# Optimization experiments

Hardware: AMD Instinct MI355X
Metric: run time of the kernel (lower is better)

## Reference

```python
import jax, jax.numpy as jnp
import numpy as np


def apply_rope(x):
    # x: [B, T, H, D]
    T, D = x.shape[1], x.shape[3]
    inv_freq = 1.0 / (10000.0 ** (jnp.arange(0, D, 2, dtype=jnp.float32) / D))  # [D/2]
    t = jnp.arange(T, dtype=jnp.float32)
    freqs = jnp.outer(t, inv_freq)  # [T, D/2]
    sin_f = jnp.sin(freqs)[None, :, None, :]
    cos_f = jnp.cos(freqs)[None, :, None, :]
    x1, x2 = jnp.split(x, 2, axis=-1)
    return jnp.concatenate([x1 * cos_f - x2 * sin_f, x1 * sin_f + x2 * cos_f], axis=-1)


def setup_inputs() -> dict:
    key = jax.random.key(0)
    ks = jax.random.split(key, 5)
    B, T, D = 8, 8192, 128
    s = 1.0 / np.sqrt(D)
    return {
        "x": jax.random.normal(ks[0], (B, T, D), dtype=jnp.float32),
        "Wq": jax.random.normal(ks[1], (D, D), dtype=jnp.float32) * s,
        "bq": jnp.zeros((D,), dtype=jnp.float32),
        "Wk": jax.random.normal(ks[2], (D, D), dtype=jnp.float32) * s,
        "bk": jnp.zeros((D,), dtype=jnp.float32),
        "Wv": jax.random.normal(ks[3], (D, D), dtype=jnp.float32) * s,
        "bv": jnp.zeros((D,), dtype=jnp.float32),
        "Wo": jax.random.normal(ks[4], (D, D), dtype=jnp.float32) * s,
        "bo": jnp.zeros((D,), dtype=jnp.float32),
    }


def reference(x, Wq, bq, Wk, bk, Wv, bv, Wo, bo):
    n_heads = 8
    B, T, d_model = x.shape
    head_dim = d_model // n_heads

    q = (x @ Wq + bq).reshape(B, T, n_heads, head_dim)
    k = (x @ Wk + bk).reshape(B, T, n_heads, head_dim)
    v = (x @ Wv + bv).reshape(B, T, n_heads, head_dim)

    q = jax.nn.elu(apply_rope(q)) + 1.0
    k = jax.nn.elu(apply_rope(k)) + 1.0

    # non-causal linear attention: context = sum_t k_t v_t^T per head
    context = jnp.einsum("bthd,bthe->bhde", k, v)            # [B,H,Dh,Dh]
    out = jnp.einsum("bthd,bhde->bthe", q, context)           # [B,T,H,Dh]
    k_sum = jnp.sum(k, axis=1)                                  # [B,H,Dh]
    z = 1.0 / (jnp.einsum("bthd,bhd->bth", q, k_sum) + 1e-6)  # [B,T,H]
    out = out * z[..., None]

    out = out.reshape(B, T, d_model)
    return out @ Wo + bo
```

## Files before the change

### kernel.cpp

```cpp
#include <hip/hip_runtime.h>
#include <hip/hip_bf16.h>


typedef __attribute__((ext_vector_type(8))) short short8;
typedef __attribute__((ext_vector_type(4))) float floatx4;

#define DEV __device__ __forceinline__
#define MFMA __builtin_amdgcn_mfma_f32_16x16x32_bf16

DEV unsigned short bfh(float f) {
  unsigned int x = __float_as_uint(f);
  x += 0x7fffu + ((x >> 16) & 1u);
  return (unsigned short)(x >> 16);
}
DEV float bfdec(unsigned short u) { return __uint_as_float(((unsigned int)u) << 16); }
DEV void splitf(float f, unsigned short& h, unsigned short& l) {
  h = bfh(f);
  l = bfh(f - bfdec(h));
}

DEV void xpose_frag(floatx4 m0, floatx4 m1, int lane16, int quad,
                    short8& hi, short8& lo) {
  union { short8 s; unsigned short u[8]; } H, L;
#pragma unroll
  for (int j = 0; j < 8; ++j) {
    int srcLane = lane16 + (((quad & 1) * 2 + (j >> 2)) << 4);
    float vA = __shfl(m0[j & 3], srcLane, 64);
    float vB = __shfl(m1[j & 3], srcLane, 64);
    float v = (quad < 2) ? vA : vB;
    splitf(v, H.u[j], L.u[j]);
  }
  hi = H.s; lo = L.s;
}

__global__ void k_prep(const float* __restrict__ Wq, const float* __restrict__ Wk,
                       const float* __restrict__ Wv,
                       unsigned short* __restrict__ WTh, unsigned short* __restrict__ WTl,
                       float* __restrict__ ctxz, float2* __restrict__ ropeT) {
  int gid = blockIdx.x * 256 + threadIdx.x;
  if (gid < 6144) {
    int mat = gid >> 11, r = gid & 2047, n = r >> 4, k0 = (r & 15) * 8;
    const float* W = (mat == 0) ? Wq : (mat == 1) ? Wk : Wv;
    union { uint4 q; unsigned short u[8]; } oh, ol;
#pragma unroll
    for (int i = 0; i < 8; ++i) splitf(W[(size_t)(k0 + i) * 128 + n], oh.u[i], ol.u[i]);
    *(uint4*)&WTh[mat * 16384 + n * 128 + k0] = oh.q;
    *(uint4*)&WTl[mat * 16384 + n * 128 + k0] = ol.q;
  } else if (gid < 6144 + 17408) {
    ctxz[gid - 6144] = 0.0f;
  } else if (gid < 6144 + 17408 + 65536) {
    int r = gid - 23552;
    int t = r >> 3, j = r & 7;
    float invf = 1.0f / powf(10000.0f, (float)j * 0.125f);
    float s, c;
    sincosf((float)t * invf, &s, &c);
    ropeT[r] = make_float2(c, s);
  }
}

__global__ __launch_bounds__(512) void k_qkv(
    const float* __restrict__ x, const float2* __restrict__ ropeT,
    const unsigned short* __restrict__ WTh, const unsigned short* __restrict__ WTl,
    const float* __restrict__ bq, const float* __restrict__ bk, const float* __restrict__ bv,
    float* __restrict__ ctx, float* __restrict__ ksum,
    unsigned short* __restrict__ qws) {
  __shared__ unsigned short xh[64 * 136];
  __shared__ float rc[64][9], rs[64][9];
  const int tid = threadIdx.x;
  const int row0 = blockIdx.x * 64;
  const int b = row0 >> 13;
  const int t0 = row0 & 8191;

  {
    int r = tid >> 3, j = tid & 7;
    float2 cs = ropeT[(t0 + r) * 8 + j];
    rc[r][j] = cs.x; rs[r][j] = cs.y;
  }
  {
    int r = tid >> 3, cg = (tid & 7) * 16;
    const float* xp = x + (size_t)(row0 + r) * 128 + cg;
    float4 a = *(const float4*)xp;
    float4 b4 = *(const float4*)(xp + 4);
    float4 c4 = *(const float4*)(xp + 8);
    float4 d4 = *(const float4*)(xp + 12);
    float v[16] = {a.x, a.y, a.z, a.w, b4.x, b4.y, b4.z, b4.w,
                   c4.x, c4.y, c4.z, c4.w, d4.x, d4.y, d4.z, d4.w};
    union { short8 s; unsigned short u[8]; } h0, h1;
#pragma unroll
    for (int i = 0; i < 8; ++i) { h0.u[i] = bfh(v[i]); h1.u[i] = bfh(v[8 + i]); }
    *(short8*)&xh[r * 136 + cg] = h0.s;
    *(short8*)&xh[r * 136 + cg + 8] = h1.s;
  }
  __syncthreads();

  const int l = tid & 63, w = tid >> 6;
  const int lane16 = l & 15, quad = l >> 4;

  floatx4 acc[3][4];
#pragma unroll
  for (int i = 0; i < 3; ++i)
#pragma unroll
    for (int j = 0; j < 4; ++j) acc[i][j] = (floatx4){0.f, 0.f, 0.f, 0.f};

  size_t wbase[3];
#pragma unroll
  for (int mat = 0; mat < 3; ++mat)
    wbase[mat] = (size_t)mat * 16384 + (size_t)(w * 16 + lane16) * 128 + quad * 8;

  short8 wh[2][3], wl[2][3];
#pragma unroll
  for (int mat = 0; mat < 3; ++mat) {
    wh[0][mat] = *(const short8*)(WTh + wbase[mat]);
    wl[0][mat] = *(const short8*)(WTl + wbase[mat]);
  }

#pragma unroll
  for (int ks = 0; ks < 4; ++ks) {
    const int cur = ks & 1, nxt = cur ^ 1;
    if (ks < 3) {
#pragma unroll
      for (int mat = 0; mat < 3; ++mat) {
        wh[nxt][mat] = *(const short8*)(WTh + wbase[mat] + (ks + 1) * 32);
        wl[nxt][mat] = *(const short8*)(WTl + wbase[mat] + (ks + 1) * 32);
      }
    }
    short8 afh[4];
#pragma unroll
    for (int mt = 0; mt < 4; ++mt)
      afh[mt] = *(const short8*)&xh[(mt * 16 + lane16) * 136 + ks * 32 + quad * 8];
#pragma unroll
    for (int mat = 0; mat < 3; ++mat) {
#pragma unroll
      for (int mt = 0; mt < 4; ++mt) {
        acc[mat][mt] = MFMA(afh[mt], wh[cur][mat], acc[mat][mt], 0, 0, 0);
        acc[mat][mt] = MFMA(afh[mt], wl[cur][mat], acc[mat][mt], 0, 0, 0);
      }
    }
  }

  {
    int col = w * 16 + lane16;
    float bias[3] = {bq[col], bk[col], bv[col]};
#pragma unroll
    for (int mat = 0; mat < 3; ++mat)
#pragma unroll
      for (int mt = 0; mt < 4; ++mt)
#pragma unroll
        for (int r = 0; r < 4; ++r) acc[mat][mt][r] += bias[mat];
  }

  {
    const int d = lane16, j = d & 7;
#pragma unroll
    for (int mt = 0; mt < 4; ++mt) {
      float cc[4], ss[4];
#pragma unroll
      for (int r = 0; r < 4; ++r) {
        int tl = mt * 16 + quad * 4 + r;
        cc[r] = rc[tl][j]; ss[r] = rs[tl][j];
      }
#pragma unroll
      for (int mat = 0; mat < 2; ++mat) {
#pragma unroll
        for (int r = 0; r < 4; ++r) {
          float v = acc[mat][mt][r];
          float p = __shfl_xor(v, 8);
          float nv = (d < 8) ? (v * cc[r] - p * ss[r]) : (p * ss[r] + v * cc[r]);
          acc[mat][mt][r] = (nv > 0.f) ? (nv + 1.f) : __expf(nv);
        }
      }
    }
  }
  __syncthreads();

  unsigned short* qS = xh;
#pragma unroll
  for (int mt = 0; mt < 4; ++mt)
#pragma unroll
    for (int r = 0; r < 4; ++r)
      qS[(mt * 16 + quad * 4 + r) * 136 + w * 16 + lane16] = bfh(acc[0][mt][r]);

  {
    float s = 0.f;
#pragma unroll
    for (int mt = 0; mt < 4; ++mt)
#pragma unroll
      for (int r = 0; r < 4; ++r) s += acc[1][mt][r];
    s += __shfl_xor(s, 16);
    s += __shfl_xor(s, 32);
    if (l < 16) atomicAdd(&ksum[(b * 8 + w) * 16 + lane16], s);
  }

  {
    floatx4 c = (floatx4){0.f, 0.f, 0.f, 0.f};
#pragma unroll
    for (int ks2 = 0; ks2 < 2; ++ks2) {
      short8 kh, kl, vh, vl;
      xpose_frag(acc[1][ks2 * 2], acc[1][ks2 * 2 + 1], lane16, quad, kh, kl);
      xpose_frag(acc[2][ks2 * 2], acc[2][ks2 * 2 + 1], lane16, quad, vh, vl);
      c = MFMA(kh, vh, c, 0, 0, 0);
      c = MFMA(kl, vh, c, 0, 0, 0);
      c = MFMA(kh, vl, c, 0, 0, 0);
    }
#pragma unroll
    for (int r = 0; r < 4; ++r)
      atomicAdd(&ctx[((size_t)(b * 8 + w) * 16 + quad * 4 + r) * 16 + lane16], c[r]);
  }
  __syncthreads();

  {
    int r = tid >> 3, c = (tid & 7) * 16;
    uint4 a0 = *(const uint4*)&qS[r * 136 + c];
    uint4 a1 = *(const uint4*)&qS[r * 136 + c + 8];
    *(uint4*)&qws[(size_t)(row0 + r) * 128 + c] = a0;
    *(uint4*)&qws[(size_t)(row0 + r) * 128 + c + 8] = a1;
  }
}

__global__ __launch_bounds__(512) void k_zout(
    const unsigned short* __restrict__ qws,
    const float* __restrict__ Wo, const float* __restrict__ bo,
    const float* __restrict__ ctx, const float* __restrict__ ksum,
    float* __restrict__ out) {
  __shared__ __align__(16) unsigned short mh[16384], ml[16384];
  __shared__ float ctxS[2048];
  __shared__ float ksumS[128], boS[128];
  const int tid = threadIdx.x;
  const int row0 = blockIdx.x * 128;
  const int b = row0 >> 13;
  const int l = tid & 63, w = tid >> 6;
  const int lane16 = l & 15, quad = l >> 4;

  {
    float4 c4 = *(const float4*)(ctx + (size_t)b * 2048 + tid * 4);
    *(float4*)&ctxS[tid * 4] = c4;
  }
  if (tid < 128) ksumS[tid] = ksum[b * 128 + tid];
  else if (tid < 256) boS[tid - 128] = bo[tid - 128];
  __syncthreads();

  {
    int oc = tid & 127;
    int qcg0 = (tid >> 7) * 4;
#pragma unroll
    for (int hh = 0; hh < 2; ++hh) {
      int h = (qcg0 >> 1) + hh;
      float m0[8] = {0, 0, 0, 0, 0, 0, 0, 0};
      float m1[8] = {0, 0, 0, 0, 0, 0, 0, 0};
#pragma unroll 4
      for (int e = 0; e < 16; ++e) {
        float wv = Wo[(size_t)(h * 16 + e) * 128 + oc];
        const float* cp = ctxS + h * 256 + e;
#pragma unroll
        for (int i = 0; i < 8; ++i) {
          m0[i] += cp[i * 16] * wv;
          m1[i] += cp[(8 + i) * 16] * wv;
        }
      }
#pragma unroll
      for (int half = 0; half < 2; ++half) {
        int qcg = qcg0 + hh * 2 + half;
        const float* mm = half ? m1 : m0;
        union { uint4 q; unsigned short u[8]; } oh, ol;
#pragma unroll
        for (int i = 0; i < 8; ++i) splitf(mm[i], oh.u[i], ol.u[i]);
        int grp = (((oc >> 4) * 4 + (qcg >> 2)) * 64) + (qcg & 3) * 16 + (oc & 15);
        *(uint4*)&mh[grp * 8] = oh.q;
        *(uint4*)&ml[grp * 8] = ol.q;
      }
    }
  }
  __syncthreads();

  const int trow = row0 + w * 16 + lane16;
  short8 ah[4], al[4];
#pragma unroll
  for (int ks = 0; ks < 4; ++ks) {
    union { short8 s8; unsigned short u[8]; } qq;
    qq.s8 = *(const short8*)&qws[(size_t)trow * 128 + ks * 32 + quad * 8];
    int kb = ks * 32 + quad * 8;
    float s = 0.f;
#pragma unroll
    for (int j = 0; j < 8; ++j) s += bfdec(qq.u[j]) * ksumS[kb + j];
    s += __shfl_xor(s, 16);
    float z = 1.0f / (s + 1e-6f);
    union { short8 s8; unsigned short u[8]; } H, L;
#pragma unroll
    for (int j = 0; j < 8; ++j) splitf(bfdec(qq.u[j]) * z, H.u[j], L.u[j]);
    ah[ks] = H.s8;
    al[ks] = L.s8;
  }

  floatx4 oacc[8];
#pragma unroll
  for (int j = 0; j < 8; ++j) oacc[j] = (floatx4){0.f, 0.f, 0.f, 0.f};

#pragma unroll
  for (int nt = 0; nt < 8; ++nt) {
#pragma unroll
    for (int ks = 0; ks < 4; ++ks) {
      int moff = ((nt * 4 + ks) * 64 + l) * 8;
      short8 wbh = *(const short8*)&mh[moff];
      short8 wbl = *(const short8*)&ml[moff];
      oacc[nt] = MFMA(ah[ks], wbh, oacc[nt], 0, 0, 0);
      oacc[nt] = MFMA(al[ks], wbh, oacc[nt], 0, 0, 0);
      oacc[nt] = MFMA(ah[ks], wbl, oacc[nt], 0, 0, 0);
    }
  }
  __syncthreads();

  float* outW = (float*)((char*)mh + w * 8192);
#pragma unroll
  for (int nt = 0; nt < 8; ++nt) {
    float bb = boS[nt * 16 + lane16];
#pragma unroll
    for (int r = 0; r < 4; ++r)
      outW[(quad * 4 + r) * 128 + nt * 16 + lane16] = oacc[nt][r] + bb;
  }
  __syncthreads();

  {
    int rr = l >> 2, c0 = (l & 3) * 4;
#pragma unroll
    for (int j = 0; j < 8; ++j) {
      float4 v4 = *(const float4*)&outW[rr * 128 + c0 + j * 16];
      *(float4*)&out[(size_t)(row0 + w * 16 + rr) * 128 + c0 + j * 16] = v4;
    }
  }
}

extern "C" void kernel_launch(void* const* d_in, const int* in_sizes, int n_in,
                              void* d_out, int out_size, void* d_ws, size_t ws_size,
                              hipStream_t stream) {
  const float* x  = (const float*)d_in[0];
  const float* Wq = (const float*)d_in[1];
  const float* bq = (const float*)d_in[2];
  const float* Wk = (const float*)d_in[3];
  const float* bk = (const float*)d_in[4];
  const float* Wv = (const float*)d_in[5];
  const float* bv = (const float*)d_in[6];
  const float* Wo = (const float*)d_in[7];
  const float* bo = (const float*)d_in[8];
  float* out = (float*)d_out;

  unsigned short* qws = (unsigned short*)d_ws;
  unsigned short* WTh = qws + 8388608;
  unsigned short* WTl = WTh + 49152;
  float* ctx  = (float*)(WTl + 49152);
  float* ksum = ctx + 16384;
  float2* ropeT = (float2*)(ksum + 1024);

  k_prep<<<348, 256, 0, stream>>>(Wq, Wk, Wv, WTh, WTl, ctx, ropeT);
  k_qkv<<<1024, 512, 0, stream>>>(x, ropeT, WTh, WTl, bq, bk, bv, ctx, ksum, qws);
  k_zout<<<512, 512, 0, stream>>>(qws, Wo, bo, ctx, ksum, out);
}
```

Measured before the change: 164.0 us.

## Fuse QKV and output kernels into one cooperative kernel with grid barrier

Merges the QKV/context kernel and the output-projection kernel into one cooperatively launched kernel of 256 blocks. Each block handles 256 rows in four 64-row tiles. Q is kept in shared memory rather than written to a bf16 workspace and read back, and ctx/ksum partials are accumulated in registers across tiles, so each block issues one set of atomics. A global atomic barrier separates the context reduction from the output phase. In exchange, grid parallelism is reduced, tiles are processed serially, shared memory use grows, and the code now depends on cooperative launch and the barrier counter being zeroed by k_prep.

Result: slower. 229.8 us (+40.1%).

```diff
diff --git a/kernel.cpp b/kernel.cpp
--- a/kernel.cpp
+++ b/kernel.cpp
@@ -46,10 +46,10 @@
     for (int i = 0; i < 8; ++i) splitf(W[(size_t)(k0 + i) * 128 + n], oh.u[i], ol.u[i]);
     *(uint4*)&WTh[mat * 16384 + n * 128 + k0] = oh.q;
     *(uint4*)&WTl[mat * 16384 + n * 128 + k0] = ol.q;
-  } else if (gid < 6144 + 17408) {
+  } else if (gid < 6144 + 17424) {
     ctxz[gid - 6144] = 0.0f;
-  } else if (gid < 6144 + 17408 + 65536) {
-    int r = gid - 23552;
+  } else if (gid < 6144 + 17424 + 65536) {
+    int r = gid - 23568;
     int t = r >> 3, j = r & 7;
     float invf = 1.0f / powf(10000.0f, (float)j * 0.125f);
     float s, c;
@@ -58,185 +58,174 @@
   }
 }
 
-__global__ __launch_bounds__(512) void k_qkv(
+__global__ __launch_bounds__(512, 2) void k_main(
     const float* __restrict__ x, const float2* __restrict__ ropeT,
     const unsigned short* __restrict__ WTh, const unsigned short* __restrict__ WTl,
     const float* __restrict__ bq, const float* __restrict__ bk, const float* __restrict__ bv,
-    float* __restrict__ ctx, float* __restrict__ ksum,
-    unsigned short* __restrict__ qws) {
-  __shared__ unsigned short xh[64 * 136];
-  __shared__ float rc[64][9], rs[64][9];
+    const float* __restrict__ Wo, const float* __restrict__ bo,
+    float* __restrict__ ctx, float* __restrict__ ksum, unsigned int* __restrict__ bar,
+    float* __restrict__ out) {
+  __shared__ unsigned short qS[256 * 136];
+  __shared__ union {
+    struct { unsigned short xh[64 * 136]; float rc[64][9]; float rs[64][9]; } p1;
+    struct { unsigned short mh[16384], ml[16384];
+             float ctxS[2048], ksumS[128], boS[128]; } p2;
+  } U;
   const int tid = threadIdx.x;
-  const int row0 = blockIdx.x * 64;
+  const int row0 = blockIdx.x * 256;
   const int b = row0 >> 13;
-  const int t0 = row0 & 8191;
-
-  {
-    int r = tid >> 3, j = tid & 7;
-    float2 cs = ropeT[(t0 + r) * 8 + j];
-    rc[r][j] = cs.x; rs[r][j] = cs.y;
-  }
-  {
-    int r = tid >> 3, cg = (tid & 7) * 16;
-    const float* xp = x + (size_t)(row0 + r) * 128 + cg;
-    float4 a = *(const float4*)xp;
-    float4 b4 = *(const float4*)(xp + 4);
-    float4 c4 = *(const float4*)(xp + 8);
-    float4 d4 = *(const float4*)(xp + 12);
-    float v[16] = {a.x, a.y, a.z, a.w, b4.x, b4.y, b4.z, b4.w,
-                   c4.x, c4.y, c4.z, c4.w, d4.x, d4.y, d4.z, d4.w};
-    union { short8 s; unsigned short u[8]; } h0, h1;
-#pragma unroll
-    for (int i = 0; i < 8; ++i) { h0.u[i] = bfh(v[i]); h1.u[i] = bfh(v[8 + i]); }
-    *(short8*)&xh[r * 136 + cg] = h0.s;
-    *(short8*)&xh[r * 136 + cg + 8] = h1.s;
-  }
-  __syncthreads();
-
   const int l = tid & 63, w = tid >> 6;
   const int lane16 = l & 15, quad = l >> 4;
 
-  floatx4 acc[3][4];
-#pragma unroll
-  for (int i = 0; i < 3; ++i)
-#pragma unroll
-    for (int j = 0; j < 4; ++j) acc[i][j] = (floatx4){0.f, 0.f, 0.f, 0.f};
-
-  size_t wbase[3];
-#pragma unroll
-  for (int mat = 0; mat < 3; ++mat)
-    wbase[mat] = (size_t)mat * 16384 + (size_t)(w * 16 + lane16) * 128 + quad * 8;
-
-  short8 wh[2][3], wl[2][3];
-#pragma unroll
-  for (int mat = 0; mat < 3; ++mat) {
-    wh[0][mat] = *(const short8*)(WTh + wbase[mat]);
-    wl[0][mat] = *(const short8*)(WTl + wbase[mat]);
-  }
-
-#pragma unroll
-  for (int ks = 0; ks < 4; ++ks) {
-    const int cur = ks & 1, nxt = cur ^ 1;
-    if (ks < 3) {
-#pragma unroll
-      for (int mat = 0; mat < 3; ++mat) {
-        wh[nxt][mat] = *(const short8*)(WTh + wbase[mat] + (ks + 1) * 32);
-        wl[nxt][mat] = *(const short8*)(WTl + wbase[mat] + (ks + 1) * 32);
-      }
-    }
-    short8 afh[4];
+  short8 wfh[4][3], wfl[4][3];
+#pragma unroll
+  for (int ks = 0; ks < 4; ++ks)
+#pragma unroll
+    for (int mat = 0; mat < 3; ++mat) {
+      size_t off = (size_t)mat * 16384 + (size_t)(w * 16 + lane16) * 128 + ks * 32 + quad * 8;
+      wfh[ks][mat] = *(const short8*)(WTh + off);
+      wfl[ks][mat] = *(const short8*)(WTl + off);
+    }
+  const int col = w * 16 + lane16;
+  const float biasq = bq[col], biask = bk[col], biasv = bv[col];
+
+  float ksum_acc = 0.f;
+  floatx4 ctxc = (floatx4){0.f, 0.f, 0.f, 0.f};
+
+#pragma unroll 1
+  for (int tile = 0; tile < 4; ++tile) {
+    const int trow0 = row0 + tile * 64;
+    const int t0 = trow0 & 8191;
+    {
+      int r = tid >> 3, j = tid & 7;
+      float2 cs = ropeT[(t0 + r) * 8 + j];
+      U.p1.rc[r][j] = cs.x; U.p1.rs[r][j] = cs.y;
+    }
+    {
+      int r = tid >> 3, cg = (tid & 7) * 16;
+      const float* xp = x + (size_t)(trow0 + r) * 128 + cg;
+      float4 a = *(const float4*)xp;
+      float4 b4 = *(const float4*)(xp + 4);
+      float4 c4 = *(const float4*)(xp + 8);
+      float4 d4 = *(const float4*)(xp + 12);
+      float v[16] = {a.x, a.y, a.z, a.w, b4.x, b4.y, b4.z, b4.w,
+                     c4.x, c4.y, c4.z, c4.w, d4.x, d4.y, d4.z, d4.w};
+      union { short8 s; unsigned short u[8]; } h0, h1;
+#pragma unroll
+      for (int i = 0; i < 8; ++i) { h0.u[i] = bfh(v[i]); h1.u[i] = bfh(v[8 + i]); }
+      *(short8*)&U.p1.xh[r * 136 + cg] = h0.s;
+      *(short8*)&U.p1.xh[r * 136 + cg + 8] = h1.s;
+    }
+    __syncthreads();
+
+    floatx4 acc[3][4];
+#pragma unroll
+    for (int i = 0; i < 3; ++i)
+#pragma unroll
+      for (int j = 0; j < 4; ++j) acc[i][j] = (floatx4){0.f, 0.f, 0.f, 0.f};
+
+#pragma unroll
+    for (int ks = 0; ks < 4; ++ks) {
+      short8 afh[4];
+#pragma unroll
+      for (int mt = 0; mt < 4; ++mt)
+        afh[mt] = *(const short8*)&U.p1.xh[(mt * 16 + lane16) * 136 + ks * 32 + quad * 8];
+#pragma unroll
+      for (int mat = 0; mat < 3; ++mat)
+#pragma unroll
+        for (int mt = 0; mt < 4; ++mt) {
+          acc[mat][mt] = MFMA(afh[mt], wfh[ks][mat], acc[mat][mt], 0, 0, 0);
+          acc[mat][mt] = MFMA(afh[mt], wfl[ks][mat], acc[mat][mt], 0, 0, 0);
+        }
+    }
+
 #pragma unroll
     for (int mt = 0; mt < 4; ++mt)
-      afh[mt] = *(const short8*)&xh[(mt * 16 + lane16) * 136 + ks * 32 + quad * 8];
-#pragma unroll
-    for (int mat = 0; mat < 3; ++mat) {
+#pragma unroll
+      for (int r = 0; r < 4; ++r) {
+        acc[0][mt][r] += biasq; acc[1][mt][r] += biask; acc[2][mt][r] += biasv;
+      }
+
+    {
+      const int d = lane16, j = d & 7;
 #pragma unroll
       for (int mt = 0; mt < 4; ++mt) {
-        acc[mat][mt] = MFMA(afh[mt], wh[cur][mat], acc[mat][mt], 0, 0, 0);
-        acc[mat][mt] = MFMA(afh[mt], wl[cur][mat], acc[mat][mt], 0, 0, 0);
-      }
-    }
-  }
-
-  {
-    int col = w * 16 + lane16;
-    float bias[3] = {bq[col], bk[col], bv[col]};
-#pragma unroll
-    for (int mat = 0; mat < 3; ++mat)
-#pragma unroll
-      for (int mt = 0; mt < 4; ++mt)
-#pragma unroll
-        for (int r = 0; r < 4; ++r) acc[mat][mt][r] += bias[mat];
-  }
-
-  {
-    const int d = lane16, j = d & 7;
-#pragma unroll
-    for (int mt = 0; mt < 4; ++mt) {
-      float cc[4], ss[4];
-#pragma unroll
-      for (int r = 0; r < 4; ++r) {
-        int tl = mt * 16 + quad * 4 + r;
-        cc[r] = rc[tl][j]; ss[r] = rs[tl][j];
-      }
-#pragma unroll
-      for (int mat = 0; mat < 2; ++mat) {
+        float cc[4], ss[4];
 #pragma unroll
         for (int r = 0; r < 4; ++r) {
-          float v = acc[mat][mt][r];
-          float p = __shfl_xor(v, 8);
-          float nv = (d < 8) ? (v * cc[r] - p * ss[r]) : (p * ss[r] + v * cc[r]);
-          acc[mat][mt][r] = (nv > 0.f) ? (nv + 1.f) : __expf(nv);
+          int tl = mt * 16 + quad * 4 + r;
+          cc[r] = U.p1.rc[tl][j]; ss[r] = U.p1.rs[tl][j];
         }
-      }
-    }
-  }
-  __syncthreads();
-
-  unsigned short* qS = xh;
-#pragma unroll
-  for (int mt = 0; mt < 4; ++mt)
-#pragma unroll
-    for (int r = 0; r < 4; ++r)
-      qS[(mt * 16 + quad * 4 + r) * 136 + w * 16 + lane16] = bfh(acc[0][mt][r]);
-
-  {
-    float s = 0.f;
+#pragma unroll
+        for (int mat = 0; mat < 2; ++mat)
+#pragma unroll
+          for (int r = 0; r < 4; ++r) {
+            float v = acc[mat][mt][r];
+            float p = __shfl_xor(v, 8);
+            float nv = (d < 8) ? (v * cc[r] - p * ss[r]) : (p * ss[r] + v * cc[r]);
+            acc[mat][mt][r] = (nv > 0.f) ? (nv + 1.f) : __expf(nv);
+          }
+      }
+    }
+
 #pragma unroll
     for (int mt = 0; mt < 4; ++mt)
 #pragma unroll
-      for (int r = 0; r < 4; ++r) s += acc[1][mt][r];
-    s += __shfl_xor(s, 16);
-    s += __shfl_xor(s, 32);
-    if (l < 16) atomicAdd(&ksum[(b * 8 + w) * 16 + lane16], s);
-  }
-
-  {
-    floatx4 c = (floatx4){0.f, 0.f, 0.f, 0.f};
+      for (int r = 0; r < 4; ++r)
+        qS[(tile * 64 + mt * 16 + quad * 4 + r) * 136 + col] = bfh(acc[0][mt][r]);
+
+#pragma unroll
+    for (int mt = 0; mt < 4; ++mt)
+#pragma unroll
+      for (int r = 0; r < 4; ++r) ksum_acc += acc[1][mt][r];
+
 #pragma unroll
     for (int ks2 = 0; ks2 < 2; ++ks2) {
       short8 kh, kl, vh, vl;
       xpose_frag(acc[1][ks2 * 2], acc[1][ks2 * 2 + 1], lane16, quad, kh, kl);
       xpose_frag(acc[2][ks2 * 2], acc[2][ks2 * 2 + 1], lane16, quad, vh, vl);
-      c = MFMA(kh, vh, c, 0, 0, 0);
-      c = MFMA(kl, vh, c, 0, 0, 0);
-      c = MFMA(kh, vl, c, 0, 0, 0);
-    }
-#pragma unroll
-    for (int r = 0; r < 4; ++r)
-      atomicAdd(&ctx[((size_t)(b * 8 + w) * 16 + quad * 4 + r) * 16 + lane16], c[r]);
-  }
+      ctxc = MFMA(kh, vh, ctxc, 0, 0, 0);
+      ctxc = MFMA(kl, vh, ctxc, 0, 0, 0);
+      ctxc = MFMA(kh, vl, ctxc, 0, 0, 0);
+    }
+    __syncthreads();
+  }
+
+  {
+    float s = ksum_acc;
+    s += __shfl_xor(s, 16);
+    s += __shfl_xor(s, 32);
+    if (l < 16) atomicAdd(&ksum[(b * 8 + w) * 16 + lane16], s);
+  }
+#pragma unroll
+  for (int r = 0; r < 4; ++r)
+    atomicAdd(&ctx[((size_t)(b * 8 + w) * 16 + quad * 4 + r) * 16 + lane16], ctxc[r]);
+
+  __threadfence();
   __syncthreads();
+  if (tid == 0) {
+    unsigned arrived =
+        __hip_atomic_fetch_add(bar, 1u, __ATOMIC_ACQ_REL, __HIP_MEMORY_SCOPE_AGENT) + 1u;
+    if (arrived == gridDim.x) {
+      __hip_atomic_store(bar + 1, 1u, __ATOMIC_RELEASE, __HIP_MEMORY_SCOPE_AGENT);
+    } else {
+      while (__hip_atomic_load(bar + 1, __ATOMIC_ACQUIRE, __HIP_MEMORY_SCOPE_AGENT) == 0u)
+        __builtin_amdgcn_s_sleep(32);
+    }
+  }
+  __syncthreads();
 
   {
-    int r = tid >> 3, c = (tid & 7) * 16;
-    uint4 a0 = *(const uint4*)&qS[r * 136 + c];
-    uint4 a1 = *(const uint4*)&qS[r * 136 + c + 8];
-    *(uint4*)&qws[(size_t)(row0 + r) * 128 + c] = a0;
-    *(uint4*)&qws[(size_t)(row0 + r) * 128 + c + 8] = a1;
-  }
-}
-
-__global__ __launch_bounds__(512) void k_zout(
-    const unsigned short* __restrict__ qws,
-    const float* __restrict__ Wo, const float* __restrict__ bo,
-    const float* __restrict__ ctx, const float* __restrict__ ksum,
-    float* __restrict__ out) {
-  __shared__ __align__(16) unsigned short mh[16384], ml[16384];
-  __shared__ float ctxS[2048];
-  __shared__ float ksumS[128], boS[128];
-  const int tid = threadIdx.x;
-  const int row0 = blockIdx.x * 128;
-  const int b = row0 >> 13;
-  const int l = tid & 63, w = tid >> 6;
-  const int lane16 = l & 15, quad = l >> 4;
-
-  {
-    float4 c4 = *(const float4*)(ctx + (size_t)b * 2048 + tid * 4);
-    *(float4*)&ctxS[tid * 4] = c4;
-  }
-  if (tid < 128) ksumS[tid] = ksum[b * 128 + tid];
-  else if (tid < 256) boS[tid - 128] = bo[tid - 128];
+#pragma unroll
+    for (int i = 0; i < 4; ++i)
+      U.p2.ctxS[tid * 4 + i] = __hip_atomic_load(&ctx[(size_t)b * 2048 + tid * 4 + i],
+                                                 __ATOMIC_RELAXED, __HIP_MEMORY_SCOPE_AGENT);
+    if (tid < 128)
+      U.p2.ksumS[tid] = __hip_atomic_load(&ksum[b * 128 + tid],
+                                          __ATOMIC_RELAXED, __HIP_MEMORY_SCOPE_AGENT);
+    else if (tid < 256)
+      U.p2.boS[tid - 128] = bo[tid - 128];
+  }
   __syncthreads();
 
   {
@@ -250,7 +239,7 @@
 #pragma unroll 4
       for (int e = 0; e < 16; ++e) {
         float wv = Wo[(size_t)(h * 16 + e) * 128 + oc];
-        const float* cp = ctxS + h * 256 + e;
+        const float* cp = U.p2.ctxS + h * 256 + e;
 #pragma unroll
         for (int i = 0; i < 8; ++i) {
           m0[i] += cp[i * 16] * wv;
@@ -265,66 +254,58 @@
 #pragma unroll
         for (int i = 0; i < 8; ++i) splitf(mm[i], oh.u[i], ol.u[i]);
         int grp = (((oc >> 4) * 4 + (qcg >> 2)) * 64) + (qcg & 3) * 16 + (oc & 15);
-        *(uint4*)&mh[grp * 8] = oh.q;
-        *(uint4*)&ml[grp * 8] = ol.q;
+        *(uint4*)&U.p2.mh[grp * 8] = oh.q;
+        *(uint4*)&U.p2.ml[grp * 8] = ol.q;
       }
     }
   }
   __syncthreads();
 
-  const int trow = row0 + w * 16 + lane16;
-  short8 ah[4], al[4];
-#pragma unroll
-  for (int ks = 0; ks < 4; ++ks) {
-    union { short8 s8; unsigned short u[8]; } qq;
-    qq.s8 = *(const short8*)&qws[(size_t)trow * 128 + ks * 32 + quad * 8];
-    int kb = ks * 32 + quad * 8;
-    float s = 0.f;
-#pragma unroll
-    for (int j = 0; j < 8; ++j) s += bfdec(qq.u[j]) * ksumS[kb + j];
-    s += __shfl_xor(s, 16);
-    float z = 1.0f / (s + 1e-6f);
-    union { short8 s8; unsigned short u[8]; } H, L;
-#pragma unroll
-    for (int j = 0; j < 8; ++j) splitf(bfdec(qq.u[j]) * z, H.u[j], L.u[j]);
-    ah[ks] = H.s8;
-    al[ks] = L.s8;
-  }
-
-  floatx4 oacc[8];
-#pragma unroll
-  for (int j = 0; j < 8; ++j) oacc[j] = (floatx4){0.f, 0.f, 0.f, 0.f};
-
-#pragma unroll
-  for (int nt = 0; nt < 8; ++nt) {
+#pragma unroll
+  for (int mt2 = 0; mt2 < 2; ++mt2) {
+    const int trowL = w * 32 + mt2 * 16 + lane16;
+    short8 ah[4], al[4];
 #pragma unroll
     for (int ks = 0; ks < 4; ++ks) {
-      int moff = ((nt * 4 + ks) * 64 + l) * 8;
-      short8 wbh = *(const short8*)&mh[moff];
-      short8 wbl = *(const short8*)&ml[moff];
-      oacc[nt] = MFMA(ah[ks], wbh, oacc[nt], 0, 0, 0);
-      oacc[nt] = MFMA(al[ks], wbh, oacc[nt], 0, 0, 0);
-      oacc[nt] = MFMA(ah[ks], wbl, oacc[nt], 0, 0, 0);
-    }
-  }
-  __syncthreads();
-
-  float* outW = (float*)((char*)mh + w * 8192);
-#pragma unroll
-  for (int nt = 0; nt < 8; ++nt) {
-    float bb = boS[nt * 16 + lane16];
-#pragma unroll
-    for (int r = 0; r < 4; ++r)
-      outW[(quad * 4 + r) * 128 + nt * 16 + lane16] = oacc[nt][r] + bb;
-  }
-  __syncthreads();
-
-  {
-    int rr = l >> 2, c0 = (l & 3) * 4;
-#pragma unroll
-    for (int j = 0; j < 8; ++j) {
-      float4 v4 = *(const float4*)&outW[rr * 128 + c0 + j * 16];
-      *(float4*)&out[(size_t)(row0 + w * 16 + rr) * 128 + c0 + j * 16] = v4;
+      union { short8 s8; unsigned short u[8]; } qq;
+      qq.s8 = *(const short8*)&qS[trowL * 136 + ks * 32 + quad * 8];
+      int kb = ks * 32 + quad * 8;
+      float s = 0.f;
+#pragma unroll
+      for (int j = 0; j < 8; ++j) s += bfdec(qq.u[j]) * U.p2.ksumS[kb + j];
+      s += __shfl_xor(s, 16);
+      float z = 1.0f / (s + 1e-6f);
+      union { short8 s8; unsigned short u[8]; } H, L;
+#pragma unroll
+      for (int j = 0; j < 8; ++j) splitf(bfdec(qq.u[j]) * z, H.u[j], L.u[j]);
+      ah[ks] = H.s8;
+      al[ks] = L.s8;
+    }
+
+    floatx4 oacc[8];
+#pragma unroll
+    for (int j = 0; j < 8; ++j) oacc[j] = (floatx4){0.f, 0.f, 0.f, 0.f};
+#pragma unroll
+    for (int nt = 0; nt < 8; ++nt)
+#pragma unroll
+      for (int ks = 0; ks < 4; ++ks) {
+        int moff = ((nt * 4 + ks) * 64 + l) * 8;
+        short8 wbh = *(const short8*)&U.p2.mh[moff];
+        short8 wbl = *(const short8*)&U.p2.ml[moff];
+        oacc[nt] = MFMA(ah[ks], wbh, oacc[nt], 0, 0, 0);
+        oacc[nt] = MFMA(al[ks], wbh, oacc[nt], 0, 0, 0);
+        oacc[nt] = MFMA(ah[ks], wbl, oacc[nt], 0, 0, 0);
+      }
+
+#pragma unroll
+    for (int nt = 0; nt < 8; ++nt) {
+      int oc = nt * 16 + lane16;
+      float bb = U.p2.boS[oc];
+#pragma unroll
+      for (int r = 0; r < 4; ++r) {
+        int t = row0 + w * 32 + mt2 * 16 + quad * 4 + r;
+        out[(size_t)t * 128 + oc] = oacc[nt][r] + bb;
+      }
     }
   }
 }
@@ -343,14 +324,17 @@
   const float* bo = (const float*)d_in[8];
   float* out = (float*)d_out;
 
-  unsigned short* qws = (unsigned short*)d_ws;
-  unsigned short* WTh = qws + 8388608;
+  unsigned short* WTh = (unsigned short*)d_ws;
   unsigned short* WTl = WTh + 49152;
   float* ctx  = (float*)(WTl + 49152);
   float* ksum = ctx + 16384;
-  float2* ropeT = (float2*)(ksum + 1024);
-
-  k_prep<<<348, 256, 0, stream>>>(Wq, Wk, Wv, WTh, WTl, ctx, ropeT);
-  k_qkv<<<1024, 512, 0, stream>>>(x, ropeT, WTh, WTl, bq, bk, bv, ctx, ksum, qws);
-  k_zout<<<512, 512, 0, stream>>>(qws, Wo, bo, ctx, ksum, out);
-}
+  unsigned int* bar = (unsigned int*)(ksum + 1024);
+  float2* ropeT = (float2*)((float*)bar + 16);
+
+  k_prep<<<349, 256, 0, stream>>>(Wq, Wk, Wv, WTh, WTl, ctx, ropeT);
+
+  void* args[] = {(void*)&x, (void*)&ropeT, (void*)&WTh, (void*)&WTl,
+                  (void*)&bq, (void*)&bk, (void*)&bv, (void*)&Wo, (void*)&bo,
+                  (void*)&ctx, (void*)&ksum, (void*)&bar, (void*)&out};
+  hipLaunchCooperativeKernel((const void*)k_main, dim3(256), dim3(512), args, 0, stream);
+}
```
